# Optimization experiments

Measured on AMD Instinct MI355X. Metric: run time of the kernel, lower is better.

The kernel has to match this reference:

```python
import jax, jax.numpy as jnp
import numpy as np

WIN = 11      # window_size in pytorch_msssim
SIGMA = 1.5   # gaussian sigma in create_window
LEVELS = 5


def _gauss_window(channels, dtype):
    # 1D gaussian -> normalized 2D window, replicated per channel for depthwise conv
    x = jnp.arange(WIN, dtype=dtype) - WIN // 2
    g = jnp.exp(-(x * x) / (2.0 * SIGMA * SIGMA))
    g = g / jnp.sum(g)
    w2 = jnp.outer(g, g)  # [11,11]
    return jnp.broadcast_to(w2[None, None], (channels, 1, WIN, WIN))


def _dwconv(x, w):
    # depthwise valid conv, NCHW (matches F.conv2d(..., padding=0, groups=channel))
    return jax.lax.conv_general_dilated(
        x, w, window_strides=(1, 1), padding='VALID',
        dimension_numbers=('NCHW', 'OIHW', 'NCHW'),
        feature_group_count=x.shape[1])


def _ssim_cs(p, t, w):
    # pytorch_msssim.ssim with full=True, val_range L=1 (inputs in [0,1])
    C1 = 0.01 ** 2
    C2 = 0.03 ** 2
    mu1 = _dwconv(p, w)
    mu2 = _dwconv(t, w)
    mu1_sq = mu1 * mu1
    mu2_sq = mu2 * mu2
    mu1_mu2 = mu1 * mu2
    sigma1_sq = _dwconv(p * p, w) - mu1_sq
    sigma2_sq = _dwconv(t * t, w) - mu2_sq
    sigma12 = _dwconv(p * t, w) - mu1_mu2
    v1 = 2.0 * sigma12 + C2
    v2 = sigma1_sq + sigma2_sq + C2
    # per-category means (axis 1 = the 10 categories, batched as channels)
    cs = jnp.mean(v1 / v2, axis=(0, 2, 3))                                   # [C]
    sim = jnp.mean(((2.0 * mu1_mu2 + C1) * v1) / ((mu1_sq + mu2_sq + C1) * v2),
                   axis=(0, 2, 3))                                           # [C]
    return sim, cs


def _avg_pool2(x):
    n, c, h, w = x.shape
    return x.reshape(n, c, h // 2, 2, w // 2, 2).mean(axis=(3, 5))


def setup_inputs() -> dict:
    key = jax.random.key(0)
    k1, k2 = jax.random.split(key)
    y_pred = jax.random.uniform(k1, (10, 1024, 1024), dtype=jnp.float32)
    y_true = jax.random.uniform(k2, (10, 1024, 1024), dtype=jnp.float32)
    return {"y_pred": y_pred, "y_true": y_true}


def reference(y_pred, y_true):
    # MSSLoss.forward: loss = sum over 10 categories of msssim(pred[c], true[c]);
    # return 1 - mean(loss)  (loss is a scalar, so mean is identity).
    # All 10 per-category msssim calls are batched as channels of one depthwise conv.
    dtype = y_pred.dtype
    weights = jnp.array([0.0448, 0.2856, 0.3001, 0.2363, 0.1333], dtype=dtype)
    p = y_pred[None]  # [1,10,H,W]
    t = y_true[None]
    w = _gauss_window(p.shape[1], dtype)
    sims, css = [], []
    for _ in range(LEVELS):
        s, c = _ssim_cs(p, t, w)
        sims.append(s)
        css.append(c)
        p = _avg_pool2(p)
        t = _avg_pool2(t)
    mssim = jnp.stack(sims)  # [5, 10]
    mcs = jnp.stack(css)     # [5, 10]
    pow1 = mcs ** weights[:, None]
    pow2 = mssim ** weights[:, None]
    # Po-Hsun-Su pytorch_msssim: output = torch.prod(pow1[:-1] * pow2[-1])
    per_cat = jnp.prod(pow1[:-1] * pow2[-1][None, :], axis=0)  # [10]
    return 1.0 - jnp.sum(per_cat)
```

## Files before the change

### kernel.cpp

```cpp
#include <hip/hip_runtime.h>
#include <cstddef>

#define WIN 11
#define HALO 10
#define NCH 10

typedef float v4f __attribute__((ext_vector_type(4)));

constexpr float Gc[WIN] = {
    0.00102838f, 0.00759876f, 0.03600077f, 0.10936069f, 0.21300554f,
    0.26601173f, 0.21300554f, 0.10936069f, 0.03600077f, 0.00759876f,
    0.00102838f};

constexpr int HPITCH = 33;
constexpr int RS = 42;
constexpr int RSZ = RS * HPITCH;

struct Ptrs {
    const float* p[5];
    const float* t[5];
};

__global__ __launch_bounds__(256) void pool_all(
    const float* __restrict__ P0, const float* __restrict__ T0,
    float* __restrict__ p1, float* __restrict__ t1,
    float* __restrict__ p2, float* __restrict__ t2,
    float* __restrict__ p3, float* __restrict__ t3,
    float* __restrict__ p4, float* __restrict__ t4,
    float* __restrict__ acc) {
    __shared__ float sp2[256], st2[256], sp3[64], st3[64];
    const int tid = threadIdx.x;
    if (blockIdx.x == 0 && tid < 128) acc[tid] = 0.f;

    const int b = blockIdx.x;
    const int bx = b & 15, by = (b >> 4) & 15, ch = b >> 8;
    const int tx = tid & 15, ty = tid >> 4;

    const size_t rbase =
        ((size_t)ch * 1024 + by * 64 + ty * 4) * 1024 + bx * 64 + tx * 4;
    float4 pr[4], tr[4];
#pragma unroll
    for (int r2 = 0; r2 < 4; ++r2) {
        pr[r2] = *(const float4*)(P0 + rbase + (size_t)r2 * 1024);
        tr[r2] = *(const float4*)(T0 + rbase + (size_t)r2 * 1024);
    }
    float p1a = 0.25f * ((pr[0].x + pr[0].y) + (pr[1].x + pr[1].y));
    float p1b = 0.25f * ((pr[0].z + pr[0].w) + (pr[1].z + pr[1].w));
    float p1c = 0.25f * ((pr[2].x + pr[2].y) + (pr[3].x + pr[3].y));
    float p1d = 0.25f * ((pr[2].z + pr[2].w) + (pr[3].z + pr[3].w));
    float t1a = 0.25f * ((tr[0].x + tr[0].y) + (tr[1].x + tr[1].y));
    float t1b = 0.25f * ((tr[0].z + tr[0].w) + (tr[1].z + tr[1].w));
    float t1c = 0.25f * ((tr[2].x + tr[2].y) + (tr[3].x + tr[3].y));
    float t1d = 0.25f * ((tr[2].z + tr[2].w) + (tr[3].z + tr[3].w));
    size_t o1 = ((size_t)ch * 512 + by * 32 + ty * 2) * 512 + bx * 32 + tx * 2;
    *(float2*)(p1 + o1) = make_float2(p1a, p1b);
    *(float2*)(p1 + o1 + 512) = make_float2(p1c, p1d);
    *(float2*)(t1 + o1) = make_float2(t1a, t1b);
    *(float2*)(t1 + o1 + 512) = make_float2(t1c, t1d);
    float p2v = 0.25f * ((p1a + p1b) + (p1c + p1d));
    float t2v = 0.25f * ((t1a + t1b) + (t1c + t1d));
    size_t o2 = ((size_t)ch * 256 + by * 16 + ty) * 256 + bx * 16 + tx;
    p2[o2] = p2v;
    t2[o2] = t2v;
    sp2[tid] = p2v;
    st2[tid] = t2v;
    __syncthreads();
    if (tid < 64) {
        int x3 = tid & 7, y3 = tid >> 3;
        int i0 = (2 * y3) * 16 + 2 * x3;
        float p3v = 0.25f * ((sp2[i0] + sp2[i0 + 1]) + (sp2[i0 + 16] + sp2[i0 + 17]));
        float t3v = 0.25f * ((st2[i0] + st2[i0 + 1]) + (st2[i0 + 16] + st2[i0 + 17]));
        size_t o3 = ((size_t)ch * 128 + by * 8 + y3) * 128 + bx * 8 + x3;
        p3[o3] = p3v;
        t3[o3] = t3v;
        sp3[tid] = p3v;
        st3[tid] = t3v;
    }
    __syncthreads();
    if (tid < 16) {
        int x4 = tid & 3, y4 = tid >> 2;
        int i0 = (2 * y4) * 8 + 2 * x4;
        float p4v = 0.25f * ((sp3[i0] + sp3[i0 + 1]) + (sp3[i0 + 8] + sp3[i0 + 9]));
        float t4v = 0.25f * ((st3[i0] + st3[i0 + 1]) + (st3[i0 + 8] + st3[i0 + 9]));
        size_t o4 = ((size_t)ch * 64 + by * 4 + y4) * 64 + bx * 4 + x4;
        p4[o4] = p4v;
        t4[o4] = t4v;
    }
}

struct V14 {
    float4 a, b, c;
    float2 d;
};

__device__ __forceinline__ float v14el(const V14& v, int j) {
    switch (j) {
        case 0:  return v.a.x;
        case 1:  return v.a.y;
        case 2:  return v.a.z;
        case 3:  return v.a.w;
        case 4:  return v.b.x;
        case 5:  return v.b.y;
        case 6:  return v.b.z;
        case 7:  return v.b.w;
        case 8:  return v.c.x;
        case 9:  return v.c.y;
        case 10: return v.c.z;
        case 11: return v.c.w;
        case 12: return v.d.x;
        default: return v.d.y;
    }
}

__device__ __forceinline__ void loadV14(const float* R, int rem, V14& v) {
    if (rem >= 14) {
        v.a = *(const float4*)R;
        v.b = *(const float4*)(R + 4);
        v.c = *(const float4*)(R + 8);
        v.d = *(const float2*)(R + 12);
    } else {
        v.a.x = (rem > 0) ? R[0] : 0.f;
        v.a.y = (rem > 1) ? R[1] : 0.f;
        v.a.z = (rem > 2) ? R[2] : 0.f;
        v.a.w = (rem > 3) ? R[3] : 0.f;
        v.b.x = (rem > 4) ? R[4] : 0.f;
        v.b.y = (rem > 5) ? R[5] : 0.f;
        v.b.z = (rem > 6) ? R[6] : 0.f;
        v.b.w = (rem > 7) ? R[7] : 0.f;
        v.c.x = (rem > 8) ? R[8] : 0.f;
        v.c.y = (rem > 9) ? R[9] : 0.f;
        v.c.z = (rem > 10) ? R[10] : 0.f;
        v.c.w = (rem > 11) ? R[11] : 0.f;
        v.d.x = (rem > 12) ? R[12] : 0.f;
        v.d.y = 0.f;
    }
}

__device__ __forceinline__ void conv2(const V14& p, const V14& t, int jbase,
                                      v4f& o0, v4f& o1) {
    v4f a0 = (v4f){0.f, 0.f, 0.f, 0.f};
    v4f a1 = a0;
#pragma unroll
    for (int u = 0; u < 12; ++u) {
        float pv = v14el(p, jbase + u);
        float tv = v14el(t, jbase + u);
        v4f xq = (v4f){pv, tv, pv * pv + tv * tv, pv * tv};
        if (u <= 10) a0 += Gc[u] * xq;
        if (u >= 1)  a1 += Gc[u - 1] * xq;
    }
    o0 = a0;
    o1 = a1;
}

__device__ __forceinline__ void conv_store4(v4f* __restrict__ hq, int rr, int x0,
                                            const V14& p, const V14& t) {
    const int sb = rr * HPITCH + x0;
    v4f o0, o1;
    conv2(p, t, 0, o0, o1);
    hq[sb + 0] = o0;
    hq[sb + 1] = o1;
    conv2(p, t, 2, o0, o1);
    hq[sb + 2] = o0;
    hq[sb + 3] = o1;
}

__global__ __launch_bounds__(256, 8) void ssim_strip(Ptrs ptrs,
                                                     float* __restrict__ acc) {
    __shared__ v4f hq[RSZ];
    __shared__ float red[8];

    const int bxi = blockIdx.x;
    int lvl, base;
    if (bxi < 128)      { lvl = 0; base = 0; }
    else if (bxi < 160) { lvl = 1; base = 128; }
    else if (bxi < 168) { lvl = 2; base = 160; }
    else if (bxi < 172) { lvl = 3; base = 168; }
    else                { lvl = 4; base = 172; }
    const int local = bxi - base;
    const int H = 1024 >> lvl;
    const int Wout = H - HALO;
    const int ncol = 32 >> lvl;
    const int cs = local & (ncol - 1);
    const int rsi = local >> (5 - lvl);
    const int X0 = cs * 32;
    const int strip_y0 = rsi * 256;
    const int strip_rows = min(256, Wout - strip_y0);
    const int rows_needed = strip_rows + HALO;
    const int nIter = (strip_rows + 15) >> 4;

    const int c = blockIdx.y;
    const float* Pc = ptrs.p[lvl] + (size_t)c * H * H;
    const float* Tc = ptrs.t[lvl] + (size_t)c * H * H;
    const int tid = threadIdx.x;

    {
        const int r = tid >> 3, seg = tid & 7;
        if (r < 26) {
            const int gxb = X0 + 4 * seg;
            const int rem = H - gxb;
            const size_t ro = (size_t)(strip_y0 + r) * H + gxb;
            V14 p, t;
            loadV14(Pc + ro, rem, p);
            loadV14(Tc + ro, rem, t);
            conv_store4(hq, r, 4 * seg, p, t);
        }
    }

    const bool isProd = (tid >= 128);
    const int idx = tid & 127;
    const int prow = (idx & 7) | ((idx >> 6) << 3);
    const int pseg = (idx >> 3) & 7;
    const int pgxb = X0 + 4 * pseg;
    const int prem = H - pgxb;
    const float* Pp = Pc + (size_t)(strip_y0 + 26 + prow) * H + pgxb;
    const float* Tp = Tc + (size_t)(strip_y0 + 26 + prow) * H + pgxb;
    V14 pp, pt;
    int prSlot = 26 + prow;
    int prRowRel = 26 + prow;
    bool pHave = false;
    if (isProd) {
        loadV14(Pp, prem, pp);
        loadV14(Tp, prem, pt);
        pHave = true;
    }
    __syncthreads();

    float cs_sum = 0.f, sim_sum = 0.f;
    const int txl = tid & 31;
    const int g = (tid >> 5) & 3;
    int y0m = 0;
    for (int i = 0; i < nIter; ++i) {
        if (isProd) {
            if (pHave) conv_store4(hq, prSlot, 4 * pseg, pp, pt);
            prSlot += 16;
            if (prSlot >= RS) prSlot -= RS;
            prRowRel += 16;
            Pp += (size_t)16 * H;
            Tp += (size_t)16 * H;
            pHave = (prRowRel < rows_needed) && (i + 2 < nIter);
            if (pHave) {
                loadV14(Pp, prem, pp);
                loadV14(Tp, prem, pt);
            }
        } else {
            int sl = y0m + 4 * g;
            if (sl >= RS) sl -= RS;
            int ad = sl * HPITCH + txl;
            v4f a0 = (v4f){0.f, 0.f, 0.f, 0.f};
            v4f a1 = a0, a2 = a0, a3 = a0;
#pragma unroll
            for (int j = 0; j < 14; ++j) {
                v4f vq = hq[ad];
                if (j <= 10)           a0 += Gc[j] * vq;
                if (j >= 1 && j <= 11) a1 += Gc[j - 1] * vq;
                if (j >= 2 && j <= 12) a2 += Gc[j - 2] * vq;
                if (j >= 3)            a3 += Gc[j - 3] * vq;
                ad += HPITCH;
                ++sl;
                if (sl >= RS) { sl = 0; ad -= RSZ; }
            }
            const float C1c = 1.0e-4f, C2c = 9.0e-4f;
            const bool colok = (X0 + txl) < Wout;
            const int orow0 = 16 * i + 4 * g;
            auto emit = [&](const v4f& av, int o) {
                if (colok && (orow0 + o) < strip_rows) {
                    float mu1 = av.x, mu2 = av.y;
                    float mu1s = mu1 * mu1, mu2s = mu2 * mu2, mu12 = mu1 * mu2;
                    float v2 = av.z - mu1s - mu2s + C2c;
                    float v1 = 2.f * (av.w - mu12) + C2c;
                    float den2 = mu1s + mu2s + C1c;
                    float num2 = 2.f * mu12 + C1c;
                    float inv = 1.f / (v2 * den2);
                    cs_sum = fmaf(v1 * den2, inv, cs_sum);
                    sim_sum = fmaf(num2 * v1, inv, sim_sum);
                }
            };
            emit(a0, 0);
            emit(a1, 1);
            emit(a2, 2);
            emit(a3, 3);
        }
        y0m += 16;
        if (y0m >= RS) y0m -= RS;
        __syncthreads();
    }

#pragma unroll
    for (int off = 32; off > 0; off >>= 1) {
        cs_sum += __shfl_down(cs_sum, off, 64);
        sim_sum += __shfl_down(sim_sum, off, 64);
    }
    int wave = tid >> 6;
    if ((tid & 63) == 0) {
        red[wave * 2 + 0] = sim_sum;
        red[wave * 2 + 1] = cs_sum;
    }
    __syncthreads();
    if (tid == 0) {
        float s = red[0] + red[2] + red[4] + red[6];
        float cc = red[1] + red[3] + red[5] + red[7];
        atomicAdd(&acc[(lvl * NCH + c) * 2 + 0], s);
        atomicAdd(&acc[(lvl * NCH + c) * 2 + 1], cc);
    }
}

__global__ void finalize_k(const float* __restrict__ acc, float* __restrict__ out) {
    if (threadIdx.x != 0) return;
    const double w[5] = {0.0448, 0.2856, 0.3001, 0.2363, 0.1333};
    const double counts[5] = {1014.0 * 1014.0, 502.0 * 502.0, 246.0 * 246.0,
                              118.0 * 118.0, 54.0 * 54.0};
    double total = 0.0;
    for (int c = 0; c < NCH; ++c) {
        double pc = 1.0;
        for (int l = 0; l < 4; ++l) {
            double mcs = (double)acc[(l * NCH + c) * 2 + 1] / counts[l];
            pc *= pow(mcs, w[l]);
        }
        double ms4 = (double)acc[(4 * NCH + c) * 2 + 0] / counts[4];
        double p2 = pow(ms4, w[4]);
        pc *= (p2 * p2) * (p2 * p2);
        total += pc;
    }
    *out = (float)(1.0 - total);
}

extern "C" void kernel_launch(void* const* d_in, const int* in_sizes, int n_in,
                              void* d_out, int out_size, void* d_ws, size_t ws_size,
                              hipStream_t stream) {
    const float* P0 = (const float*)d_in[0];
    const float* T0 = (const float*)d_in[1];
    float* out = (float*)d_out;
    float* acc = (float*)d_ws;

    const size_t n1 = (size_t)NCH * 512 * 512;
    const size_t n2 = (size_t)NCH * 256 * 256;
    const size_t n3 = (size_t)NCH * 128 * 128;
    const size_t n4 = (size_t)NCH * 64 * 64;
    float* p1 = acc + 128;
    float* t1 = p1 + n1;
    float* p2 = t1 + n1;
    float* t2 = p2 + n2;
    float* p3 = t2 + n2;
    float* t3 = p3 + n3;
    float* p4 = t3 + n3;
    float* t4 = p4 + n4;

    pool_all<<<2560, 256, 0, stream>>>(P0, T0, p1, t1, p2, t2, p3, t3, p4, t4, acc);

    Ptrs ptrs;
    ptrs.p[0] = P0; ptrs.t[0] = T0;
    ptrs.p[1] = p1; ptrs.t[1] = t1;
    ptrs.p[2] = p2; ptrs.t[2] = t2;
    ptrs.p[3] = p3; ptrs.t[3] = t3;
    ptrs.p[4] = p4; ptrs.t[4] = t4;

    ssim_strip<<<dim3(174, NCH, 1), 256, 0, stream>>>(ptrs, acc);

    finalize_k<<<1, 64, 0, stream>>>(acc, out);
}
```

Before: 206.6 us.

## Mirror ring-buffer rows in LDS, fuse horizontal conv, use fast reciprocal

The shared ring buffer gains 13 mirror rows, so consumers read 14 consecutive rows with a fixed stride and no wraparound checks. Producers write the first rows twice. The horizontal convolution now computes four outputs in one pass instead of two pairs, and the per-output division becomes a hardware reciprocal. A fast path skips the row bounds checks for full groups. The larger LDS footprint lowers launch bounds occupancy from 8 to 5 blocks, and rcp slightly reduces precision.

```diff
diff --git a/kernel.cpp b/kernel.cpp
--- a/kernel.cpp
+++ b/kernel.cpp
@@ -14,7 +14,9 @@
 
 constexpr int HPITCH = 33;
 constexpr int RS = 42;
-constexpr int RSZ = RS * HPITCH;
+constexpr int MIR = 13;
+constexpr int RSLOTS = RS + MIR;
+constexpr int RSZ = RSLOTS * HPITCH;
 
 struct Ptrs {
     const float* p[5];
@@ -136,35 +138,35 @@
     }
 }
 
-__device__ __forceinline__ void conv2(const V14& p, const V14& t, int jbase,
-                                      v4f& o0, v4f& o1) {
-    v4f a0 = (v4f){0.f, 0.f, 0.f, 0.f};
-    v4f a1 = a0;
-#pragma unroll
-    for (int u = 0; u < 12; ++u) {
-        float pv = v14el(p, jbase + u);
-        float tv = v14el(t, jbase + u);
-        v4f xq = (v4f){pv, tv, pv * pv + tv * tv, pv * tv};
-        if (u <= 10) a0 += Gc[u] * xq;
-        if (u >= 1)  a1 += Gc[u - 1] * xq;
-    }
-    o0 = a0;
-    o1 = a1;
-}
-
 __device__ __forceinline__ void conv_store4(v4f* __restrict__ hq, int rr, int x0,
                                             const V14& p, const V14& t) {
+    v4f a0 = (v4f){0.f, 0.f, 0.f, 0.f};
+    v4f a1 = a0, a2 = a0, a3 = a0;
+#pragma unroll
+    for (int xi = 0; xi < 14; ++xi) {
+        float pv = v14el(p, xi);
+        float tv = v14el(t, xi);
+        v4f xq = (v4f){pv, tv, pv * pv + tv * tv, pv * tv};
+        if (xi <= 10)            a0 += Gc[xi] * xq;
+        if (xi >= 1 && xi <= 11) a1 += Gc[xi - 1] * xq;
+        if (xi >= 2 && xi <= 12) a2 += Gc[xi - 2] * xq;
+        if (xi >= 3)             a3 += Gc[xi - 3] * xq;
+    }
     const int sb = rr * HPITCH + x0;
-    v4f o0, o1;
-    conv2(p, t, 0, o0, o1);
-    hq[sb + 0] = o0;
-    hq[sb + 1] = o1;
-    conv2(p, t, 2, o0, o1);
-    hq[sb + 2] = o0;
-    hq[sb + 3] = o1;
-}
-
-__global__ __launch_bounds__(256, 8) void ssim_strip(Ptrs ptrs,
+    hq[sb + 0] = a0;
+    hq[sb + 1] = a1;
+    hq[sb + 2] = a2;
+    hq[sb + 3] = a3;
+    if (rr < MIR) {
+        const int mb = sb + RS * HPITCH;
+        hq[mb + 0] = a0;
+        hq[mb + 1] = a1;
+        hq[mb + 2] = a2;
+        hq[mb + 3] = a3;
+    }
+}
+
+__global__ __launch_bounds__(256, 5) void ssim_strip(Ptrs ptrs,
                                                      float* __restrict__ acc) {
     __shared__ v4f hq[RSZ];
     __shared__ float red[8];
@@ -243,42 +245,47 @@
                 loadV14(Tp, prem, pt);
             }
         } else {
-            int sl = y0m + 4 * g;
-            if (sl >= RS) sl -= RS;
-            int ad = sl * HPITCH + txl;
+            int sl0 = y0m + 4 * g;
+            if (sl0 >= RS) sl0 -= RS;
+            const int ad0 = sl0 * HPITCH + txl;
             v4f a0 = (v4f){0.f, 0.f, 0.f, 0.f};
             v4f a1 = a0, a2 = a0, a3 = a0;
 #pragma unroll
             for (int j = 0; j < 14; ++j) {
-                v4f vq = hq[ad];
+                v4f vq = hq[ad0 + j * HPITCH];
                 if (j <= 10)           a0 += Gc[j] * vq;
                 if (j >= 1 && j <= 11) a1 += Gc[j - 1] * vq;
                 if (j >= 2 && j <= 12) a2 += Gc[j - 2] * vq;
                 if (j >= 3)            a3 += Gc[j - 3] * vq;
-                ad += HPITCH;
-                ++sl;
-                if (sl >= RS) { sl = 0; ad -= RSZ; }
             }
             const float C1c = 1.0e-4f, C2c = 9.0e-4f;
             const bool colok = (X0 + txl) < Wout;
             const int orow0 = 16 * i + 4 * g;
-            auto emit = [&](const v4f& av, int o) {
-                if (colok && (orow0 + o) < strip_rows) {
-                    float mu1 = av.x, mu2 = av.y;
-                    float mu1s = mu1 * mu1, mu2s = mu2 * mu2, mu12 = mu1 * mu2;
-                    float v2 = av.z - mu1s - mu2s + C2c;
-                    float v1 = 2.f * (av.w - mu12) + C2c;
-                    float den2 = mu1s + mu2s + C1c;
-                    float num2 = 2.f * mu12 + C1c;
-                    float inv = 1.f / (v2 * den2);
-                    cs_sum = fmaf(v1 * den2, inv, cs_sum);
-                    sim_sum = fmaf(num2 * v1, inv, sim_sum);
+            auto ssim1 = [&](const v4f& av) {
+                float mu1 = av.x, mu2 = av.y;
+                float mu1s = mu1 * mu1, mu2s = mu2 * mu2, mu12 = mu1 * mu2;
+                float v2 = av.z - mu1s - mu2s + C2c;
+                float v1 = 2.f * (av.w - mu12) + C2c;
+                float den2 = mu1s + mu2s + C1c;
+                float num2 = 2.f * mu12 + C1c;
+                float den = v2 * den2;
+                float inv = __builtin_amdgcn_rcpf(den);
+                cs_sum = fmaf(v1 * den2, inv, cs_sum);
+                sim_sum = fmaf(num2 * v1, inv, sim_sum);
+            };
+            if (colok) {
+                if (orow0 + 4 <= strip_rows) {
+                    ssim1(a0);
+                    ssim1(a1);
+                    ssim1(a2);
+                    ssim1(a3);
+                } else {
+                    if (orow0 + 0 < strip_rows) ssim1(a0);
+                    if (orow0 + 1 < strip_rows) ssim1(a1);
+                    if (orow0 + 2 < strip_rows) ssim1(a2);
+                    if (orow0 + 3 < strip_rows) ssim1(a3);
                 }
-            };
-            emit(a0, 0);
-            emit(a1, 1);
-            emit(a2, 2);
-            emit(a3, 3);
+            }
         }
         y0m += 16;
         if (y0m >= RS) y0m -= RS;
```

Measured after the change: 225.0 us. 8.9% more time.
